# Optimization experiments

Measured on AMD Instinct MI355X. Metric: run time of the kernel, lower is better.

Reference implementation:

```python
import jax, jax.numpy as jnp
import numpy as np

N_ATOMS = 50000
N_EDGES = 100000
ATOM_DIM = 64
BOND_DIM = 16


def setup_inputs() -> dict:
    key = jax.random.key(0)
    k1, k2, k3, k4, k5 = jax.random.split(key, 5)
    atom_features = jax.random.normal(k1, (N_ATOMS, ATOM_DIM), dtype=jnp.float32)
    bond_features = jax.random.normal(k2, (N_EDGES, BOND_DIM), dtype=jnp.float32)
    # target indices (column 0) must be sorted for tf.math.segment_sum semantics
    tgt = jnp.sort(jax.random.randint(k3, (N_EDGES,), 0, N_ATOMS))
    nbr = jax.random.randint(k4, (N_EDGES,), 0, N_ATOMS)
    pair_indices = jnp.stack([tgt, nbr], axis=1).astype(jnp.int64)
    # glorot_uniform for kernel of shape (BOND_DIM, ATOM_DIM*ATOM_DIM)
    fan_in, fan_out = BOND_DIM, ATOM_DIM * ATOM_DIM
    limit = float(np.sqrt(6.0 / (fan_in + fan_out)))
    kernel = jax.random.uniform(k5, (BOND_DIM, ATOM_DIM * ATOM_DIM),
                                dtype=jnp.float32, minval=-limit, maxval=limit)
    bias = jnp.zeros((ATOM_DIM * ATOM_DIM,), dtype=jnp.float32)
    return {"atom_features": atom_features, "bond_features": bond_features,
            "pair_indices": pair_indices, "kernel": kernel, "bias": bias}


def reference(atom_features, bond_features, pair_indices, kernel, bias):
    n_atoms, atom_dim = atom_features.shape
    # project bond features to a per-edge [atom_dim, atom_dim] transform
    bf = bond_features @ kernel + bias            # [E, atom_dim^2]
    bf = bf.reshape(-1, atom_dim, atom_dim)       # [E, D, D]
    # gather neighbor atom features
    nbr = atom_features[pair_indices[:, 1]]       # [E, D]
    # per-edge matvec
    msg = jnp.einsum('eij,ej->ei', bf, nbr)       # [E, D]
    # scatter-reduce by target atom index
    agg = jax.ops.segment_sum(msg, pair_indices[:, 0], num_segments=n_atoms)
    return agg
```

## Files before the change

### kernel.cpp

```cpp
#include <hip/hip_runtime.h>
#include <hip/hip_bf16.h>
#include <climits>

#define NATOMS 50000
#define NEDGES 100000
#define AD 64
#define BD 16
#define PITCH 1096
#define NR ((NEDGES + 31) / 32)
#define NBANDS 256
#define NWAVES 16

typedef __bf16 bf16x8 __attribute__((ext_vector_type(8)));
typedef __bf16 bf16x4 __attribute__((ext_vector_type(4)));
typedef float  f32x16 __attribute__((ext_vector_type(16)));

__device__ __forceinline__ void first_break2(const int* __restrict__ pair,
                                             int p0, int p1, const int lane,
                                             int& s, int& e) {
    const int qa = p0 + lane;
    const int qb = p1 + lane;
    const bool ba = (qa == 0 || qa >= NEDGES) ? true : (pair[2 * qa] != pair[2 * qa - 2]);
    const bool bb = (qb == 0 || qb >= NEDGES) ? true : (pair[2 * qb] != pair[2 * qb - 2]);
    const unsigned long long ma = __ballot(ba);
    const unsigned long long mb = __ballot(bb);

    if (ma) { s = p0 + (int)__builtin_ctzll(ma); if (s > NEDGES) s = NEDGES; }
    else {
        int p = p0 + 64;
        while (true) {
            const int q = p + lane;
            const bool bk = (q >= NEDGES) ? true : (pair[2 * q] != pair[2 * q - 2]);
            const unsigned long long m = __ballot(bk);
            if (m) { s = p + (int)__builtin_ctzll(m); if (s > NEDGES) s = NEDGES; break; }
            p += 64;
        }
    }
    if (mb) { e = p1 + (int)__builtin_ctzll(mb); if (e > NEDGES) e = NEDGES; }
    else {
        int p = p1 + 64;
        while (true) {
            const int q = p + lane;
            const bool bk = (q >= NEDGES) ? true : (pair[2 * q] != pair[2 * q - 2]);
            const unsigned long long m = __ballot(bk);
            if (m) { e = p + (int)__builtin_ctzll(m); if (e > NEDGES) e = NEDGES; break; }
            p += 64;
        }
    }
}

__device__ __forceinline__ void scan_slot(
    const int g, const int e,
    const float* __restrict__ atom, const float* __restrict__ bond,
    const int* __restrict__ pair,
    const __bf16* __restrict__ Brow0, const __bf16* __restrict__ Brow1,
    const int l31, const int half, const int h8,
    f32x16& acc0, f32x16& acc1, int& myTgt, bool& isLast)
{
    const int eA = g + l31;
    const bool validE = (eA < e);
    const int eAc = validE ? eA : 0;

    int ni = pair[2 * eAc + 1];
    if ((unsigned)ni >= NATOMS) ni = 0;
    const float* nbrRow  = atom + (long)ni * AD;
    const float* bondRow = bond + (long)eAc * BD;

    float nb[4][8];
    #pragma unroll
    for (int q = 0; q < 4; ++q) {
        const float4 lo = *reinterpret_cast<const float4*>(nbrRow + q * 16 + h8);
        const float4 hi = *reinterpret_cast<const float4*>(nbrRow + q * 16 + h8 + 4);
        nb[q][0] = lo.x; nb[q][1] = lo.y; nb[q][2] = lo.z; nb[q][3] = lo.w;
        nb[q][4] = hi.x; nb[q][5] = hi.y; nb[q][6] = hi.z; nb[q][7] = hi.w;
    }
    float bd[16];
    #pragma unroll
    for (int q = 0; q < 4; ++q) {
        const float4 v = *reinterpret_cast<const float4*>(bondRow + q * 4);
        bd[q * 4 + 0] = v.x; bd[q * 4 + 1] = v.y;
        bd[q * 4 + 2] = v.z; bd[q * 4 + 3] = v.w;
    }

    #pragma unroll
    for (int r = 0; r < 16; ++r) { acc0[r] = 0.f; acc1[r] = 0.f; }

    #pragma unroll
    for (int t = 0; t < 64; ++t) {
        const float bv = bd[t >> 2];
        bf16x8 a;
        #pragma unroll
        for (int r = 0; r < 8; ++r) a[r] = (__bf16)(bv * nb[t & 3][r]);
        const int k0 = t * 16 + h8;
        const bf16x8 b0 = *reinterpret_cast<const bf16x8*>(Brow0 + k0);
        const bf16x8 b1 = *reinterpret_cast<const bf16x8*>(Brow1 + k0);
        acc0 = __builtin_amdgcn_mfma_f32_32x32x16_bf16(b0, a, acc0, 0, 0, 0);
        acc1 = __builtin_amdgcn_mfma_f32_32x32x16_bf16(b1, a, acc1, 0, 0, 0);
    }
    #pragma unroll
    for (int t = 64; t < 68; ++t) {
        bf16x8 a;
        #pragma unroll
        for (int r = 0; r < 8; ++r) a[r] = (__bf16)(nb[t - 64][r]);
        const int k0 = t * 16 + h8;
        const bf16x8 b0 = *reinterpret_cast<const bf16x8*>(Brow0 + k0);
        const bf16x8 b1 = *reinterpret_cast<const bf16x8*>(Brow1 + k0);
        acc0 = __builtin_amdgcn_mfma_f32_32x32x16_bf16(b0, a, acc0, 0, 0, 0);
        acc1 = __builtin_amdgcn_mfma_f32_32x32x16_bf16(b1, a, acc1, 0, 0, 0);
    }

    myTgt = validE ? pair[2 * eA] : INT_MAX;
    #pragma unroll
    for (int d = 1; d <= 4; d <<= 1) {
        const int srcTgt = __shfl_up(myTgt, (unsigned)d, 32);
        const bool same = (l31 >= d) && (srcTgt == myTgt);
        #pragma unroll
        for (int r = 0; r < 16; ++r) {
            const float v0 = __shfl_up(acc0[r], (unsigned)d, 32);
            const float v1 = __shfl_up(acc1[r], (unsigned)d, 32);
            if (same) { acc0[r] += v0; acc1[r] += v1; }
        }
    }
    const int src8 = __shfl_up(myTgt, 8u, 32);
    if (__any((l31 >= 8) && (src8 == myTgt))) {
        const bool same8 = (l31 >= 8) && (src8 == myTgt);
        #pragma unroll
        for (int r = 0; r < 16; ++r) {
            const float v0 = __shfl_up(acc0[r], 8u, 32);
            const float v1 = __shfl_up(acc1[r], 8u, 32);
            if (same8) { acc0[r] += v0; acc1[r] += v1; }
        }
        const int src16 = __shfl_up(myTgt, 16u, 32);
        const bool same16 = (l31 >= 16) && (src16 == myTgt);
        #pragma unroll
        for (int r = 0; r < 16; ++r) {
            const float v0 = __shfl_up(acc0[r], 16u, 32);
            const float v1 = __shfl_up(acc1[r], 16u, 32);
            if (same16) { acc0[r] += v0; acc1[r] += v1; }
        }
    }

    const int nTgt = __shfl_down(myTgt, 1u, 32);
    isLast = validE && ((l31 == 31) || (nTgt != myTgt));
}

__global__ __launch_bounds__(64 * NWAVES, 1)
void edgenet_kernel(const float* __restrict__ atom,
                    const float* __restrict__ bond,
                    const int*   __restrict__ pair,
                    const float* __restrict__ kern,
                    const float* __restrict__ bias,
                    float* __restrict__ out)
{
    __shared__ __bf16 Blds[64 * PITCH];
    __shared__ float  Trow[NWAVES][64];
    __shared__ int    Ttag[NWAVES];

    const int tid  = threadIdx.x;
    const int band = blockIdx.x;
    const int NT   = 64 * NWAVES;

    const int wave = tid >> 6;
    const int lane = tid & 63;
    const int l31  = lane & 31;
    const int half = lane >> 5;
    const int h8   = half * 8;

    for (int q = tid; q < (16 * 4096) / 4; q += NT) {
        const int idx = q * 4;
        const int b = idx >> 12;
        const int i = (idx >> 6) & 63;
        const int j = idx & 63;
        const float4 v = *reinterpret_cast<const float4*>(kern + idx);
        bf16x4 w;
        w[0] = (__bf16)v.x; w[1] = (__bf16)v.y; w[2] = (__bf16)v.z; w[3] = (__bf16)v.w;
        *reinterpret_cast<bf16x4*>(Blds + i * PITCH + (b << 6) + j) = w;
    }
    {
        const int q = tid;
        const int idx = q * 4;
        const int i = idx >> 6;
        const int j = idx & 63;
        const float4 v = *reinterpret_cast<const float4*>(bias + idx);
        bf16x4 w;
        w[0] = (__bf16)v.x; w[1] = (__bf16)v.y; w[2] = (__bf16)v.z; w[3] = (__bf16)v.w;
        *reinterpret_cast<bf16x4*>(Blds + i * PITCH + 1024 + j) = w;
    }

    const int r0 = (NR * band) / NBANDS;
    const int r1 = (NR * (band + 1)) / NBANDS;
    int sB, eB;
    first_break2(pair, 32 * r0, 32 * r1, lane, sB, eB);

    __syncthreads();

    const __bf16* __restrict__ Brow0 = Blds + l31 * PITCH;
    const __bf16* __restrict__ Brow1 = Blds + (32 + l31) * PITCH;

    const int g    = sB + 32 * wave;
    const int gEnd = (g + 32 < eB) ? (g + 32) : eB;
    const bool active = (g < eB);

    f32x16 acc0, acc1;
    int myTgt = INT_MAX;
    bool isLast = false;

    if (active) {
        scan_slot(g, gEnd, atom, bond, pair, Brow0, Brow1,
                  l31, half, h8, acc0, acc1, myTgt, isLast);
    }

    bool myContin = false;
    if (active && (l31 == 31) && (g + 32 < eB)) {
        myContin = (myTgt == pair[2 * (g + 32)]);
    }

    if (myContin) {
        #pragma unroll
        for (int r = 0; r < 16; ++r) {
            const int f = (r & 3) + 8 * (r >> 2) + 4 * half;
            Trow[wave][f]      = acc0[r];
            Trow[wave][32 + f] = acc1[r];
        }
    }
    if (lane == 31) Ttag[wave] = myContin ? myTgt : INT_MIN;

    __syncthreads();

    if (active && isLast && !myContin) {
        for (int w2 = wave - 1; w2 >= 0; --w2) {
            if (Ttag[w2] != myTgt) break;
            #pragma unroll
            for (int r = 0; r < 16; ++r) {
                const int f = (r & 3) + 8 * (r >> 2) + 4 * half;
                acc0[r] += Trow[w2][f];
                acc1[r] += Trow[w2][32 + f];
            }
        }
        float* o = out + (long)myTgt * AD;
        #pragma unroll
        for (int rq = 0; rq < 4; ++rq) {
            float4 v0, v1;
            v0.x = acc0[rq*4+0]; v0.y = acc0[rq*4+1]; v0.z = acc0[rq*4+2]; v0.w = acc0[rq*4+3];
            v1.x = acc1[rq*4+0]; v1.y = acc1[rq*4+1]; v1.z = acc1[rq*4+2]; v1.w = acc1[rq*4+3];
            *reinterpret_cast<float4*>(o + 8 * rq + 4 * half)      = v0;
            *reinterpret_cast<float4*>(o + 32 + 8 * rq + 4 * half) = v1;
        }
    }
}

extern "C" void kernel_launch(void* const* d_in, const int* in_sizes, int n_in,
                              void* d_out, int out_size, void* d_ws, size_t ws_size,
                              hipStream_t stream) {
    const float* atom = (const float*)d_in[0];
    const float* bond = (const float*)d_in[1];
    const int*   pair = (const int*)d_in[2];
    const float* kern = (const float*)d_in[3];
    const float* bias = (const float*)d_in[4];
    float* out = (float*)d_out;

    hipMemsetAsync(d_out, 0, (size_t)out_size * sizeof(float), stream);

    edgenet_kernel<<<NBANDS, 64 * NWAVES, 0, stream>>>(atom, bond, pair, kern, bias, out);
}
```

Measured before the change: 40.99 us.

## Process two 32-edge chunks per wave to reuse LDS weight loads

Halves waves per block and has each wave handle two 32-edge windows, so every bf16 weight fragment read from LDS feeds four MFMAs instead of two. Neighbor and bond loads for both chunks are issued before the barrier that follows weight staging, overlapping global latency with the kernel-to-LDS conversion. The memset is replaced by a custom zeroing kernel. This roughly doubles accumulator and input register pressure and lowers wave count per CU, which could reduce latency hiding.

```diff
diff --git a/kernel.cpp b/kernel.cpp
--- a/kernel.cpp
+++ b/kernel.cpp
@@ -9,11 +9,20 @@
 #define PITCH 1096
 #define NR ((NEDGES + 31) / 32)
 #define NBANDS 256
-#define NWAVES 16
+#define NWAVES 8
+#define NWIN (2 * NWAVES)
 
 typedef __bf16 bf16x8 __attribute__((ext_vector_type(8)));
 typedef __bf16 bf16x4 __attribute__((ext_vector_type(4)));
 typedef float  f32x16 __attribute__((ext_vector_type(16)));
+
+__global__ __launch_bounds__(256)
+void zero_out(float4* __restrict__ out, int n4) {
+    const int stride = gridDim.x * blockDim.x;
+    const float4 z = make_float4(0.f, 0.f, 0.f, 0.f);
+    for (int i = blockIdx.x * blockDim.x + threadIdx.x; i < n4; i += stride)
+        out[i] = z;
+}
 
 __device__ __forceinline__ void first_break2(const int* __restrict__ pair,
                                              int p0, int p1, const int lane,
@@ -49,13 +58,11 @@
     }
 }
 
-__device__ __forceinline__ void scan_slot(
-    const int g, const int e,
+__device__ __forceinline__ void load_chunk(
+    const int g, const int e, const int l31, const int h8,
     const float* __restrict__ atom, const float* __restrict__ bond,
     const int* __restrict__ pair,
-    const __bf16* __restrict__ Brow0, const __bf16* __restrict__ Brow1,
-    const int l31, const int half, const int h8,
-    f32x16& acc0, f32x16& acc1, int& myTgt, bool& isLast)
+    float nb[4][8], float bd[16], int& myTgt)
 {
     const int eA = g + l31;
     const bool validE = (eA < e);
@@ -66,7 +73,6 @@
     const float* nbrRow  = atom + (long)ni * AD;
     const float* bondRow = bond + (long)eAc * BD;
 
-    float nb[4][8];
     #pragma unroll
     for (int q = 0; q < 4; ++q) {
         const float4 lo = *reinterpret_cast<const float4*>(nbrRow + q * 16 + h8);
@@ -74,42 +80,18 @@
         nb[q][0] = lo.x; nb[q][1] = lo.y; nb[q][2] = lo.z; nb[q][3] = lo.w;
         nb[q][4] = hi.x; nb[q][5] = hi.y; nb[q][6] = hi.z; nb[q][7] = hi.w;
     }
-    float bd[16];
     #pragma unroll
     for (int q = 0; q < 4; ++q) {
         const float4 v = *reinterpret_cast<const float4*>(bondRow + q * 4);
         bd[q * 4 + 0] = v.x; bd[q * 4 + 1] = v.y;
         bd[q * 4 + 2] = v.z; bd[q * 4 + 3] = v.w;
     }
-
-    #pragma unroll
-    for (int r = 0; r < 16; ++r) { acc0[r] = 0.f; acc1[r] = 0.f; }
-
-    #pragma unroll
-    for (int t = 0; t < 64; ++t) {
-        const float bv = bd[t >> 2];
-        bf16x8 a;
-        #pragma unroll
-        for (int r = 0; r < 8; ++r) a[r] = (__bf16)(bv * nb[t & 3][r]);
-        const int k0 = t * 16 + h8;
-        const bf16x8 b0 = *reinterpret_cast<const bf16x8*>(Brow0 + k0);
-        const bf16x8 b1 = *reinterpret_cast<const bf16x8*>(Brow1 + k0);
-        acc0 = __builtin_amdgcn_mfma_f32_32x32x16_bf16(b0, a, acc0, 0, 0, 0);
-        acc1 = __builtin_amdgcn_mfma_f32_32x32x16_bf16(b1, a, acc1, 0, 0, 0);
-    }
-    #pragma unroll
-    for (int t = 64; t < 68; ++t) {
-        bf16x8 a;
-        #pragma unroll
-        for (int r = 0; r < 8; ++r) a[r] = (__bf16)(nb[t - 64][r]);
-        const int k0 = t * 16 + h8;
-        const bf16x8 b0 = *reinterpret_cast<const bf16x8*>(Brow0 + k0);
-        const bf16x8 b1 = *reinterpret_cast<const bf16x8*>(Brow1 + k0);
-        acc0 = __builtin_amdgcn_mfma_f32_32x32x16_bf16(b0, a, acc0, 0, 0, 0);
-        acc1 = __builtin_amdgcn_mfma_f32_32x32x16_bf16(b1, a, acc1, 0, 0, 0);
-    }
-
     myTgt = validE ? pair[2 * eA] : INT_MAX;
+}
+
+__device__ __forceinline__ bool scan_pair(
+    f32x16& acc0, f32x16& acc1, const int myTgt, const int l31, const int w)
+{
     #pragma unroll
     for (int d = 1; d <= 4; d <<= 1) {
         const int srcTgt = __shfl_up(myTgt, (unsigned)d, 32);
@@ -139,9 +121,9 @@
             if (same16) { acc0[r] += v0; acc1[r] += v1; }
         }
     }
-
     const int nTgt = __shfl_down(myTgt, 1u, 32);
-    isLast = validE && ((l31 == 31) || (nTgt != myTgt));
+    const bool validE = (l31 < w);
+    return validE && ((l31 == 31) || (nTgt != myTgt));
 }
 
 __global__ __launch_bounds__(64 * NWAVES, 1)
@@ -153,8 +135,8 @@
                     float* __restrict__ out)
 {
     __shared__ __bf16 Blds[64 * PITCH];
-    __shared__ float  Trow[NWAVES][64];
-    __shared__ int    Ttag[NWAVES];
+    __shared__ float  Trow[NWIN][64];
+    __shared__ int    Ttag[NWIN];
 
     const int tid  = threadIdx.x;
     const int band = blockIdx.x;
@@ -176,8 +158,7 @@
         w[0] = (__bf16)v.x; w[1] = (__bf16)v.y; w[2] = (__bf16)v.z; w[3] = (__bf16)v.w;
         *reinterpret_cast<bf16x4*>(Blds + i * PITCH + (b << 6) + j) = w;
     }
-    {
-        const int q = tid;
+    for (int q = tid; q < 4096 / 4; q += NT) {
         const int idx = q * 4;
         const int i = idx >> 6;
         const int j = idx & 63;
@@ -192,57 +173,129 @@
     int sB, eB;
     first_break2(pair, 32 * r0, 32 * r1, lane, sB, eB);
 
+    const int wiA = 2 * wave, wiB = 2 * wave + 1;
+    const int gA = sB + 32 * wiA;
+    const int gB = sB + 32 * wiB;
+    const int endA = (gA + 32 < eB) ? (gA + 32) : eB;
+    const int endB = (gB + 32 < eB) ? (gB + 32) : eB;
+    const bool activeA = (gA < eB);
+    const bool activeB = (gB < eB);
+    const int wA = activeA ? (endA - gA) : 0;
+    const int wB = activeB ? (endB - gB) : 0;
+
+    float nbA[4][8], bdA[16]; int tgA;
+    float nbB[4][8], bdB[16]; int tgB;
+    load_chunk(gA, endA, l31, h8, atom, bond, pair, nbA, bdA, tgA);
+    load_chunk(gB, endB, l31, h8, atom, bond, pair, nbB, bdB, tgB);
+
     __syncthreads();
 
     const __bf16* __restrict__ Brow0 = Blds + l31 * PITCH;
     const __bf16* __restrict__ Brow1 = Blds + (32 + l31) * PITCH;
 
-    const int g    = sB + 32 * wave;
-    const int gEnd = (g + 32 < eB) ? (g + 32) : eB;
-    const bool active = (g < eB);
-
-    f32x16 acc0, acc1;
-    int myTgt = INT_MAX;
-    bool isLast = false;
-
-    if (active) {
-        scan_slot(g, gEnd, atom, bond, pair, Brow0, Brow1,
-                  l31, half, h8, acc0, acc1, myTgt, isLast);
-    }
-
-    bool myContin = false;
-    if (active && (l31 == 31) && (g + 32 < eB)) {
-        myContin = (myTgt == pair[2 * (g + 32)]);
-    }
-
-    if (myContin) {
+    f32x16 aA0, aA1, aB0, aB1;
+    #pragma unroll
+    for (int r = 0; r < 16; ++r) { aA0[r]=0.f; aA1[r]=0.f; aB0[r]=0.f; aB1[r]=0.f; }
+
+    #pragma unroll
+    for (int t = 0; t < 64; ++t) {
+        const int k0 = t * 16 + h8;
+        const bf16x8 b0 = *reinterpret_cast<const bf16x8*>(Brow0 + k0);
+        const bf16x8 b1 = *reinterpret_cast<const bf16x8*>(Brow1 + k0);
+        const float bvA = bdA[t >> 2];
+        const float bvB = bdB[t >> 2];
+        bf16x8 fa, fb;
+        #pragma unroll
+        for (int r = 0; r < 8; ++r) fa[r] = (__bf16)(bvA * nbA[t & 3][r]);
+        #pragma unroll
+        for (int r = 0; r < 8; ++r) fb[r] = (__bf16)(bvB * nbB[t & 3][r]);
+        aA0 = __builtin_amdgcn_mfma_f32_32x32x16_bf16(b0, fa, aA0, 0, 0, 0);
+        aA1 = __builtin_amdgcn_mfma_f32_32x32x16_bf16(b1, fa, aA1, 0, 0, 0);
+        aB0 = __builtin_amdgcn_mfma_f32_32x32x16_bf16(b0, fb, aB0, 0, 0, 0);
+        aB1 = __builtin_amdgcn_mfma_f32_32x32x16_bf16(b1, fb, aB1, 0, 0, 0);
+    }
+    #pragma unroll
+    for (int t = 64; t < 68; ++t) {
+        const int k0 = t * 16 + h8;
+        const bf16x8 b0 = *reinterpret_cast<const bf16x8*>(Brow0 + k0);
+        const bf16x8 b1 = *reinterpret_cast<const bf16x8*>(Brow1 + k0);
+        bf16x8 fa, fb;
+        #pragma unroll
+        for (int r = 0; r < 8; ++r) fa[r] = (__bf16)(nbA[t - 64][r]);
+        #pragma unroll
+        for (int r = 0; r < 8; ++r) fb[r] = (__bf16)(nbB[t - 64][r]);
+        aA0 = __builtin_amdgcn_mfma_f32_32x32x16_bf16(b0, fa, aA0, 0, 0, 0);
+        aA1 = __builtin_amdgcn_mfma_f32_32x32x16_bf16(b1, fa, aA1, 0, 0, 0);
+        aB0 = __builtin_amdgcn_mfma_f32_32x32x16_bf16(b0, fb, aB0, 0, 0, 0);
+        aB1 = __builtin_amdgcn_mfma_f32_32x32x16_bf16(b1, fb, aB1, 0, 0, 0);
+    }
+
+    const bool lastA = scan_pair(aA0, aA1, tgA, l31, wA);
+    const bool lastB = scan_pair(aB0, aB1, tgB, l31, wB);
+
+    bool conA = false, conB = false;
+    if (activeA && (l31 == 31) && (gA + 32 < eB)) conA = (tgA == pair[2 * (gA + 32)]);
+    if (activeB && (l31 == 31) && (gB + 32 < eB)) conB = (tgB == pair[2 * (gB + 32)]);
+
+    if (conA) {
         #pragma unroll
         for (int r = 0; r < 16; ++r) {
             const int f = (r & 3) + 8 * (r >> 2) + 4 * half;
-            Trow[wave][f]      = acc0[r];
-            Trow[wave][32 + f] = acc1[r];
-        }
-    }
-    if (lane == 31) Ttag[wave] = myContin ? myTgt : INT_MIN;
+            Trow[wiA][f]      = aA0[r];
+            Trow[wiA][32 + f] = aA1[r];
+        }
+    }
+    if (conB) {
+        #pragma unroll
+        for (int r = 0; r < 16; ++r) {
+            const int f = (r & 3) + 8 * (r >> 2) + 4 * half;
+            Trow[wiB][f]      = aB0[r];
+            Trow[wiB][32 + f] = aB1[r];
+        }
+    }
+    if (lane == 31) {
+        Ttag[wiA] = conA ? tgA : INT_MIN;
+        Ttag[wiB] = conB ? tgB : INT_MIN;
+    }
 
     __syncthreads();
 
-    if (active && isLast && !myContin) {
-        for (int w2 = wave - 1; w2 >= 0; --w2) {
-            if (Ttag[w2] != myTgt) break;
+    if (activeA && lastA && !conA) {
+        for (int w2 = wiA - 1; w2 >= 0; --w2) {
+            if (Ttag[w2] != tgA) break;
             #pragma unroll
             for (int r = 0; r < 16; ++r) {
                 const int f = (r & 3) + 8 * (r >> 2) + 4 * half;
-                acc0[r] += Trow[w2][f];
-                acc1[r] += Trow[w2][32 + f];
+                aA0[r] += Trow[w2][f];
+                aA1[r] += Trow[w2][32 + f];
             }
         }
-        float* o = out + (long)myTgt * AD;
+        float* o = out + (long)tgA * AD;
         #pragma unroll
         for (int rq = 0; rq < 4; ++rq) {
             float4 v0, v1;
-            v0.x = acc0[rq*4+0]; v0.y = acc0[rq*4+1]; v0.z = acc0[rq*4+2]; v0.w = acc0[rq*4+3];
-            v1.x = acc1[rq*4+0]; v1.y = acc1[rq*4+1]; v1.z = acc1[rq*4+2]; v1.w = acc1[rq*4+3];
+            v0.x = aA0[rq*4+0]; v0.y = aA0[rq*4+1]; v0.z = aA0[rq*4+2]; v0.w = aA0[rq*4+3];
+            v1.x = aA1[rq*4+0]; v1.y = aA1[rq*4+1]; v1.z = aA1[rq*4+2]; v1.w = aA1[rq*4+3];
+            *reinterpret_cast<float4*>(o + 8 * rq + 4 * half)      = v0;
+            *reinterpret_cast<float4*>(o + 32 + 8 * rq + 4 * half) = v1;
+        }
+    }
+    if (activeB && lastB && !conB) {
+        for (int w2 = wiB - 1; w2 >= 0; --w2) {
+            if (Ttag[w2] != tgB) break;
+            #pragma unroll
+            for (int r = 0; r < 16; ++r) {
+                const int f = (r & 3) + 8 * (r >> 2) + 4 * half;
+                aB0[r] += Trow[w2][f];
+                aB1[r] += Trow[w2][32 + f];
+            }
+        }
+        float* o = out + (long)tgB * AD;
+        #pragma unroll
+        for (int rq = 0; rq < 4; ++rq) {
+            float4 v0, v1;
+            v0.x = aB0[rq*4+0]; v0.y = aB0[rq*4+1]; v0.z = aB0[rq*4+2]; v0.w = aB0[rq*4+3];
+            v1.x = aB1[rq*4+0]; v1.y = aB1[rq*4+1]; v1.z = aB1[rq*4+2]; v1.w = aB1[rq*4+3];
             *reinterpret_cast<float4*>(o + 8 * rq + 4 * half)      = v0;
             *reinterpret_cast<float4*>(o + 32 + 8 * rq + 4 * half) = v1;
         }
@@ -259,7 +312,8 @@
     const float* bias = (const float*)d_in[4];
     float* out = (float*)d_out;
 
-    hipMemsetAsync(d_out, 0, (size_t)out_size * sizeof(float), stream);
+    const int n4 = out_size / 4;
+    zero_out<<<2048, 256, 0, stream>>>((float4*)out, n4);
 
     edgenet_kernel<<<NBANDS, 64 * NWAVES, 0, stream>>>(atom, bond, pair, kern, bias, out);
 }
```

New measurement: 46.94 us. 1.14x slower.
